# Kernel optimization log

Hardware: AMD Instinct MI355X
Metric: run time of the kernel (lower is better)

## Reference

```python
import jax, jax.numpy as jnp
import numpy as np

N_NODES = 50000
N_EDGES = 800000
IN_FEATS = 128
OUT_CLASSES = 128


def _glorot(key, shape):
    fan_in, fan_out = shape[1], shape[0]
    limit = float(np.sqrt(6.0 / (fan_in + fan_out)))
    return jax.random.uniform(key, shape, jnp.float32, -limit, limit)


def setup_inputs() -> dict:
    key = jax.random.key(0)
    ks = jax.random.split(key, 11)
    x = jax.random.normal(ks[0], (N_NODES, IN_FEATS), jnp.float32)
    edge_index = jax.random.randint(ks[1], (2, N_EDGES), 0, N_NODES, jnp.int64)
    h = OUT_CLASSES // 2
    # PyG SAGEConv: lin_l applied to aggregated neighbors (has bias), lin_r to root (no bias)
    return {
        "x": x,
        "edge_index": edge_index,
        "W_l1": _glorot(ks[2], (OUT_CLASSES, IN_FEATS)),
        "b1": jnp.zeros((OUT_CLASSES,), jnp.float32),
        "W_r1": _glorot(ks[3], (OUT_CLASSES, IN_FEATS)),
        "W_l2": _glorot(ks[4], (h, OUT_CLASSES)),
        "b2": jnp.zeros((h,), jnp.float32),
        "W_r2": _glorot(ks[5], (h, OUT_CLASSES)),
        "W_l3": _glorot(ks[6], (OUT_CLASSES, h)),
        "b3": jnp.zeros((OUT_CLASSES,), jnp.float32),
        "W_r3": _glorot(ks[7], (OUT_CLASSES, h)),
    }


def _sage_conv(x, src, dst, W_l, b, W_r):
    # gather source-node features, mean-aggregate at destinations
    msgs = x[src]                                               # [E, d]
    agg = jax.ops.segment_sum(msgs, dst, num_segments=N_NODES)  # [N, d]
    cnt = jax.ops.segment_sum(jnp.ones((src.shape[0], 1), x.dtype), dst,
                              num_segments=N_NODES)             # [N, 1]
    mean = agg / jnp.maximum(cnt, 1.0)
    return mean @ W_l.T + b + x @ W_r.T


def reference(x, edge_index, W_l1, b1, W_r1, W_l2, b2, W_r2, W_l3, b3, W_r3):
    src, dst = edge_index[0], edge_index[1]
    h = _sage_conv(x, src, dst, W_l1, b1, W_r1)
    h = _sage_conv(h, src, dst, W_l2, b2, W_r2)
    h = _sage_conv(h, src, dst, W_l3, b3, W_r3)
    return h
```

## Files before the change

kernel.cpp:

```cpp
#include <hip/hip_runtime.h>

#define N_NODES 50000
#define N_EDGES 800000
#define BUCKETS 196
#define ECHUNK 4096
#define EBLKS 196
#define BCAP 5120

typedef __attribute__((ext_vector_type(8))) _Float16 half8;
typedef __attribute__((ext_vector_type(4))) float f32x4;


__global__ __launch_bounds__(256) void prep_k(
    const int* __restrict__ src, const int* __restrict__ dst,
    int* __restrict__ gcur, unsigned* __restrict__ binned,
    const float* __restrict__ x, _Float16* __restrict__ xh,
    const float* __restrict__ Wl1, const float* __restrict__ Wr1,
    const float* __restrict__ Wl2, const float* __restrict__ Wr2,
    const float* __restrict__ Wl3, const float* __restrict__ Wr3,
    _Float16* ph_l1, _Float16* pl_l1, _Float16* ph_r1, _Float16* pl_r1,
    _Float16* ph_c2, _Float16* pl_c2, _Float16* ph_l3, _Float16* pl_l3,
    _Float16* ph_r3, _Float16* pl_r3) {
  int blk = blockIdx.x;
  int t = threadIdx.x;
  if (blk < EBLKS) {
    __shared__ int h[BUCKETS];
    __shared__ int base[BUCKETS];
    for (int i = t; i < BUCKETS; i += 256) h[i] = 0;
    __syncthreads();
    int e0 = blk * ECHUNK;
    int eend = e0 + ECHUNK < N_EDGES ? e0 + ECHUNK : N_EDGES;
    for (int e = e0 + t; e < eend; e += 256) atomicAdd(&h[dst[e] >> 8], 1);
    __syncthreads();
    for (int i = t; i < BUCKETS; i += 256) {
      if (h[i]) base[i] = atomicAdd(&gcur[i], h[i]);
      h[i] = 0;
    }
    __syncthreads();
    for (int e = e0 + t; e < eend; e += 256) {
      int d = dst[e];
      int b = d >> 8;
      int r = atomicAdd(&h[b], 1);
      binned[(size_t)b * BCAP + base[b] + r] =
          (unsigned)src[e] | ((unsigned)(d & 255) << 16);
    }
  } else if (blk < EBLKS + 32) {
    int g = (blk - EBLKS) * 256 + t;
    const float *S0, *S1 = nullptr;
    _Float16 *ph, *pl;
    int f, K;
    if (g < 2048)      { f = g;        ph = ph_l1; pl = pl_l1; S0 = Wl1; K = 128; }
    else if (g < 4096) { f = g - 2048; ph = ph_r1; pl = pl_r1; S0 = Wr1; K = 128; }
    else if (g < 6144) { f = g - 4096; ph = ph_c2; pl = pl_c2; S0 = Wl2; S1 = Wr2; K = 128; }
    else if (g < 7168) { f = g - 6144; ph = ph_l3; pl = pl_l3; S0 = Wl3; K = 64; }
    else               { f = g - 7168; ph = ph_r3; pl = pl_r3; S0 = Wr3; K = 64; }
    int kb = f >> 9;
    int rem = f & 511;
    int n = rem >> 2;
    int lq = rem & 3;
    const float* srow =
        (S1 && n >= 64) ? (S1 + (size_t)(n - 64) * K) : (S0 + (size_t)n * K);
    int kbase = kb * 32 + lq * 8;
#pragma unroll
    for (int j = 0; j < 8; ++j) {
      float v = srow[kbase + j];
      _Float16 hi = (_Float16)v;
      ph[f * 8 + j] = hi;
      pl[f * 8 + j] = (_Float16)(v - (float)hi);
    }
  } else {
    int i = (blk - EBLKS - 32) * 256 + t;
    if (i >= N_NODES * 16) return;
    const float4* xp = (const float4*)x;
    float4 a = xp[2 * i];
    float4 b = xp[2 * i + 1];
    half8 hh;
    hh[0] = (_Float16)a.x; hh[1] = (_Float16)a.y; hh[2] = (_Float16)a.z; hh[3] = (_Float16)a.w;
    hh[4] = (_Float16)b.x; hh[5] = (_Float16)b.y; hh[6] = (_Float16)b.z; hh[7] = (_Float16)b.w;
    ((half8*)xh)[i] = hh;
  }
}

__global__ __launch_bounds__(256) void bucket_fill_k(const unsigned* __restrict__ binned,
                                                     const int* __restrict__ gcnt,
                                                     int* __restrict__ offs,
                                                     int* __restrict__ deg,
                                                     unsigned short* __restrict__ csr) {
  __shared__ int cnt[256];
  __shared__ int loc[256];
  __shared__ int cur[256];
  int b = blockIdx.x;
  int t = threadIdx.x;
  int base = b * BCAP;
  int end = base + gcnt[b];
  cnt[t] = 0;
  __syncthreads();
  for (int e = base + t; e < end; e += 256) atomicAdd(&cnt[(binned[e] >> 16) & 255], 1);
  __syncthreads();
  loc[t] = cnt[t];
  __syncthreads();
  for (int o = 1; o < 256; o <<= 1) {
    int v = (t >= o) ? loc[t - o] : 0;
    __syncthreads();
    loc[t] += v;
    __syncthreads();
  }
  int excl = loc[t] - cnt[t];
  int node = b * 256 + t;
  if (node < N_NODES) {
    offs[node] = base + excl;
    deg[node] = cnt[t];
  }
  cur[t] = excl;
  __syncthreads();
  for (int e = base + t; e < end; e += 256) {
    unsigned r = binned[e];
    int dl = (r >> 16) & 255;
    int p = atomicAdd(&cur[dl], 1);
    csr[base + p] = (unsigned short)(r & 0xFFFF);
  }
}


template <int D, bool FUSE>
__global__ __launch_bounds__(256) void agg_f16_k(const _Float16* __restrict__ in,
                                                 _Float16* __restrict__ out,
                                                 const int* __restrict__ offs,
                                                 const int* __restrict__ deg,
                                                 const unsigned short* __restrict__ csr,
                                                 const float* __restrict__ bias,
                                                 const _Float16* __restrict__ addend) {
  constexpr int L = D / 8;
  constexpr int NPB = 256 / L;
  int node = blockIdx.x * NPB + threadIdx.x / L;
  int lane = threadIdx.x & (L - 1);
  if (node >= N_NODES) return;
  int start = offs[node];
  int d = deg[node];
  const half8* ip = (const half8*)in;
  float acc[8];
#pragma unroll
  for (int j = 0; j < 8; ++j) acc[j] = 0.f;
  int e = 0;
  for (; e + 8 <= d; e += 8) {
    int s[8];
#pragma unroll
    for (int j = 0; j < 8; ++j) s[j] = csr[start + e + j];
    half8 v[8];
#pragma unroll
    for (int j = 0; j < 8; ++j) v[j] = ip[(size_t)s[j] * L + lane];
#pragma unroll
    for (int j = 0; j < 8; ++j)
#pragma unroll
      for (int q = 0; q < 8; ++q) acc[q] += (float)v[j][q];
  }
  for (; e + 4 <= d; e += 4) {
    int s[4];
#pragma unroll
    for (int j = 0; j < 4; ++j) s[j] = csr[start + e + j];
    half8 v[4];
#pragma unroll
    for (int j = 0; j < 4; ++j) v[j] = ip[(size_t)s[j] * L + lane];
#pragma unroll
    for (int j = 0; j < 4; ++j)
#pragma unroll
      for (int q = 0; q < 8; ++q) acc[q] += (float)v[j][q];
  }
  for (; e < d; ++e) {
    half8 v0 = ip[(size_t)csr[start + e] * L + lane];
#pragma unroll
    for (int q = 0; q < 8; ++q) acc[q] += (float)v0[q];
  }
  float inv = d > 0 ? 1.0f / (float)d : 0.0f;
  half8 o;
  if constexpr (FUSE) {
    half8 av = ((const half8*)addend)[(size_t)node * L + lane];
#pragma unroll
    for (int q = 0; q < 8; ++q)
      o[q] = (_Float16)(acc[q] * inv + bias[lane * 8 + q] + (float)av[q]);
  } else {
#pragma unroll
    for (int q = 0; q < 8; ++q) o[q] = (_Float16)(acc[q] * inv);
  }
  ((half8*)out)[(size_t)node * L + lane] = o;
}


template <int K, bool DUAL, bool SPLIT, bool OUT32>
__global__ __launch_bounds__(256, 2) void gemm_f16_k(
    const _Float16* __restrict__ A1, const _Float16* __restrict__ W1h,
    const _Float16* __restrict__ W1l,
    const _Float16* __restrict__ A2, const _Float16* __restrict__ W2h,
    const _Float16* __restrict__ W2l,
    const float* __restrict__ bias, _Float16* __restrict__ C16,
    float* __restrict__ C32, _Float16* __restrict__ O2) {
  int wave = threadIdx.x >> 6;
  int lane = threadIdx.x & 63;
  int l15 = lane & 15;
  int lq = lane >> 4;
  int rowblk = blockIdx.x >> 1;
  int colg = blockIdx.x & 1;
  int rg = rowblk * 4 + wave;
  if (rg >= N_NODES / 16) return;
  int row0 = rg << 4;
  constexpr int KB = K / 32;
  constexpr int NN = 128;
  const int woff = (l15 * 4 + lq) * 8;
  f32x4 acc[4];
#pragma unroll
  for (int c = 0; c < 4; ++c) acc[c] = (f32x4){0.f, 0.f, 0.f, 0.f};

  constexpr int NOP = DUAL ? 2 : 1;
#pragma unroll
  for (int op = 0; op < NOP; ++op) {
    const _Float16* A = op ? A2 : A1;
    const _Float16* Wh = op ? W2h : W1h;
    const _Float16* Wl = op ? W2l : W1l;
    const _Float16* ab = A + (size_t)(row0 + l15) * K + lq * 8;
    half8 af[KB];
#pragma unroll
    for (int kb = 0; kb < KB; ++kb) af[kb] = *(const half8*)(ab + kb * 32);
#pragma unroll
    for (int kb = 0; kb < KB; ++kb) {
#pragma unroll
      for (int ct = 0; ct < 4; ++ct) {
        int n0 = colg * 64 + ct * 16;
        size_t base = (size_t)(kb * NN + n0) * 32 + woff;
        half8 bh = *(const half8*)(Wh + base);
        half8 bl = *(const half8*)(Wl + base);
        acc[ct] = __builtin_amdgcn_mfma_f32_16x16x32_f16(af[kb], bh, acc[ct], 0, 0, 0);
        acc[ct] = __builtin_amdgcn_mfma_f32_16x16x32_f16(af[kb], bl, acc[ct], 0, 0, 0);
      }
    }
  }
#pragma unroll
  for (int r = 0; r < 4; ++r) {
    int row = row0 + lq * 4 + r;
#pragma unroll
    for (int ct = 0; ct < 4; ++ct) {
      int col = colg * 64 + ct * 16 + l15;
      float v = acc[ct][r];
      if constexpr (SPLIT) {
        if (col < 64)
          C16[(size_t)row * 64 + col] = (_Float16)v;
        else
          O2[(size_t)row * 64 + (col - 64)] = (_Float16)v;
      } else {
        v += bias[col];
        if constexpr (OUT32)
          C32[(size_t)row * 128 + col] = v;
        else
          C16[(size_t)row * 128 + col] = (_Float16)v;
      }
    }
  }
}

extern "C" void kernel_launch(void* const* d_in, const int* in_sizes, int n_in,
                              void* d_out, int out_size, void* d_ws, size_t ws_size,
                              hipStream_t stream) {
  const float* x   = (const float*)d_in[0];
  const int* ei    = (const int*)d_in[1];
  const float* Wl1 = (const float*)d_in[2];
  const float* b1  = (const float*)d_in[3];
  const float* Wr1 = (const float*)d_in[4];
  const float* Wl2 = (const float*)d_in[5];
  const float* b2  = (const float*)d_in[6];
  const float* Wr2 = (const float*)d_in[7];
  const float* Wl3 = (const float*)d_in[8];
  const float* b3  = (const float*)d_in[9];
  const float* Wr3 = (const float*)d_in[10];
  float* out = (float*)d_out;

  const int* src = ei;
  const int* dst = ei + N_EDGES;

  char* ws = (char*)d_ws;
  size_t off = 0;
  auto take = [&](size_t bytes) {
    void* p = ws + off;
    off += (bytes + 255) & ~(size_t)255;
    return p;
  };
  int* deg    = (int*)take((size_t)N_NODES * 4);
  int* offs   = (int*)take((size_t)N_NODES * 4);
  int* gcur   = (int*)take((size_t)BUCKETS * 4);
  unsigned* binned = (unsigned*)take((size_t)BUCKETS * BCAP * 4);
  unsigned short* csr = (unsigned short*)take((size_t)BUCKETS * BCAP * 2);
  _Float16* xh  = (_Float16*)take((size_t)N_NODES * 128 * 2);
  _Float16* m1h = (_Float16*)take((size_t)N_NODES * 128 * 2);
  _Float16* h1h = (_Float16*)take((size_t)N_NODES * 128 * 2);
  _Float16* Ph  = (_Float16*)take((size_t)N_NODES * 64 * 2);
  _Float16* Rh  = (_Float16*)take((size_t)N_NODES * 64 * 2);
  _Float16* h2h = (_Float16*)take((size_t)N_NODES * 64 * 2);
  _Float16* m3h = (_Float16*)take((size_t)N_NODES * 64 * 2);
  _Float16* ph_l1 = (_Float16*)take(16384 * 2);
  _Float16* pl_l1 = (_Float16*)take(16384 * 2);
  _Float16* ph_r1 = (_Float16*)take(16384 * 2);
  _Float16* pl_r1 = (_Float16*)take(16384 * 2);
  _Float16* ph_c2 = (_Float16*)take(16384 * 2);
  _Float16* pl_c2 = (_Float16*)take(16384 * 2);
  _Float16* ph_l3 = (_Float16*)take(8192 * 2);
  _Float16* pl_l3 = (_Float16*)take(8192 * 2);
  _Float16* ph_r3 = (_Float16*)take(8192 * 2);
  _Float16* pl_r3 = (_Float16*)take(8192 * 2);

  const int gg = 1564;

  hipMemsetAsync(gcur, 0, (size_t)BUCKETS * 4, stream);

  prep_k<<<EBLKS + 32 + 3125, 256, 0, stream>>>(
      src, dst, gcur, binned, x, xh, Wl1, Wr1, Wl2, Wr2, Wl3, Wr3, ph_l1, pl_l1,
      ph_r1, pl_r1, ph_c2, pl_c2, ph_l3, pl_l3, ph_r3, pl_r3);
  bucket_fill_k<<<BUCKETS, 256, 0, stream>>>(binned, gcur, offs, deg, csr);

  agg_f16_k<128, false><<<3125, 256, 0, stream>>>(xh, m1h, offs, deg, csr, nullptr, nullptr);
  gemm_f16_k<128, true, false, false><<<gg, 256, 0, stream>>>(
      m1h, ph_l1, pl_l1, xh, ph_r1, pl_r1, b1, h1h, nullptr, nullptr);

  gemm_f16_k<128, false, true, false><<<gg, 256, 0, stream>>>(
      h1h, ph_c2, pl_c2, nullptr, nullptr, nullptr, nullptr, Ph, nullptr, Rh);
  agg_f16_k<64, true><<<1563, 256, 0, stream>>>(Ph, h2h, offs, deg, csr, b2, Rh);

  agg_f16_k<64, false><<<1563, 256, 0, stream>>>(h2h, m3h, offs, deg, csr, nullptr, nullptr);
  gemm_f16_k<64, true, false, true><<<gg, 256, 0, stream>>>(
      m3h, ph_l3, pl_l3, h2h, ph_r3, pl_r3, b3, nullptr, out, nullptr);
}
```

Baseline: 259.2 us.

## Fuse mean aggregation into the following GEMM via shared-memory tiles for layers 1 and 3

Adds a kernel that aggregates neighbor features for a 64-node tile into LDS and then runs the dual MFMA GEMM (aggregated and root operands) for all 128 output columns in the same block. This replaces the separate aggregation kernel and GEMM kernel for layers 1 and 3, removing the m1h/m3h intermediate round-trips through global memory and two launches. In exchange, each block does gather-heavy work followed by compute, with fewer blocks (782) and less latency hiding than the separate kernels. Each wave now also computes all 128 columns rather than splitting columns across two blocks.

```diff
diff --git a/kernel.cpp b/kernel.cpp
--- a/kernel.cpp
+++ b/kernel.cpp
@@ -186,6 +186,139 @@
 }
 
 
+template <int K, bool OUT32>
+__global__ __launch_bounds__(256, 4) void fused_agg_gemm_k(
+    const _Float16* __restrict__ feat,
+    const int* __restrict__ offs, const int* __restrict__ deg,
+    const unsigned short* __restrict__ csr,
+    const _Float16* __restrict__ Wlh, const _Float16* __restrict__ Wll,
+    const _Float16* __restrict__ Wrh, const _Float16* __restrict__ Wrl,
+    const float* __restrict__ bias, _Float16* __restrict__ C16,
+    float* __restrict__ C32) {
+  constexpr int L = K / 8;
+  constexpr int CONC = 256 / L;
+  constexpr int ITER = 64 / CONC;
+  constexpr int STRIDE = K + 8;
+  constexpr int KB = K / 32;
+  __shared__ _Float16 Asm[64 * STRIDE];
+  int t = threadIdx.x;
+  int base = blockIdx.x * 64;
+  const half8* ip = (const half8*)feat;
+  {
+    int lane = t & (L - 1);
+    int slot = t / L;
+#pragma unroll
+    for (int it = 0; it < ITER; ++it) {
+      int r = it * CONC + slot;
+      int node = base + r;
+      float acc[8];
+#pragma unroll
+      for (int j = 0; j < 8; ++j) acc[j] = 0.f;
+      float inv = 0.f;
+      if (node < N_NODES) {
+        int start = offs[node];
+        int d = deg[node];
+        int e = 0;
+        for (; e + 8 <= d; e += 8) {
+          int s[8];
+#pragma unroll
+          for (int j = 0; j < 8; ++j) s[j] = csr[start + e + j];
+          half8 v[8];
+#pragma unroll
+          for (int j = 0; j < 8; ++j) v[j] = ip[(size_t)s[j] * L + lane];
+#pragma unroll
+          for (int j = 0; j < 8; ++j)
+#pragma unroll
+            for (int q = 0; q < 8; ++q) acc[q] += (float)v[j][q];
+        }
+        for (; e + 4 <= d; e += 4) {
+          int s[4];
+#pragma unroll
+          for (int j = 0; j < 4; ++j) s[j] = csr[start + e + j];
+          half8 v[4];
+#pragma unroll
+          for (int j = 0; j < 4; ++j) v[j] = ip[(size_t)s[j] * L + lane];
+#pragma unroll
+          for (int j = 0; j < 4; ++j)
+#pragma unroll
+            for (int q = 0; q < 8; ++q) acc[q] += (float)v[j][q];
+        }
+        for (; e < d; ++e) {
+          half8 v0 = ip[(size_t)csr[start + e] * L + lane];
+#pragma unroll
+          for (int q = 0; q < 8; ++q) acc[q] += (float)v0[q];
+        }
+        inv = d > 0 ? 1.0f / (float)d : 0.0f;
+      }
+      half8 o;
+#pragma unroll
+      for (int q = 0; q < 8; ++q) o[q] = (_Float16)(acc[q] * inv);
+      *(half8*)&Asm[r * STRIDE + lane * 8] = o;
+    }
+  }
+  __syncthreads();
+  int wave = t >> 6;
+  int lane = t & 63;
+  int l15 = lane & 15;
+  int lq = lane >> 4;
+  int row0 = base + wave * 16;
+  const int woff = (l15 * 4 + lq) * 8;
+  f32x4 acc[8];
+#pragma unroll
+  for (int c = 0; c < 8; ++c) acc[c] = (f32x4){0.f, 0.f, 0.f, 0.f};
+  {
+    const _Float16* asrc = &Asm[(wave * 16 + l15) * STRIDE + lq * 8];
+    half8 af[KB];
+#pragma unroll
+    for (int kb = 0; kb < KB; ++kb) af[kb] = *(const half8*)(asrc + kb * 32);
+#pragma unroll
+    for (int kb = 0; kb < KB; ++kb) {
+#pragma unroll
+      for (int ct = 0; ct < 8; ++ct) {
+        size_t bi = (size_t)(kb * 128 + ct * 16) * 32 + woff;
+        half8 bh = *(const half8*)(Wlh + bi);
+        half8 bl = *(const half8*)(Wll + bi);
+        acc[ct] = __builtin_amdgcn_mfma_f32_16x16x32_f16(af[kb], bh, acc[ct], 0, 0, 0);
+        acc[ct] = __builtin_amdgcn_mfma_f32_16x16x32_f16(af[kb], bl, acc[ct], 0, 0, 0);
+      }
+    }
+  }
+  {
+    int arow = row0 + l15;
+    if (arow >= N_NODES) arow = N_NODES - 1;
+    const _Float16* ab = feat + (size_t)arow * K + lq * 8;
+    half8 af[KB];
+#pragma unroll
+    for (int kb = 0; kb < KB; ++kb) af[kb] = *(const half8*)(ab + kb * 32);
+#pragma unroll
+    for (int kb = 0; kb < KB; ++kb) {
+#pragma unroll
+      for (int ct = 0; ct < 8; ++ct) {
+        size_t bi = (size_t)(kb * 128 + ct * 16) * 32 + woff;
+        half8 bh = *(const half8*)(Wrh + bi);
+        half8 bl = *(const half8*)(Wrl + bi);
+        acc[ct] = __builtin_amdgcn_mfma_f32_16x16x32_f16(af[kb], bh, acc[ct], 0, 0, 0);
+        acc[ct] = __builtin_amdgcn_mfma_f32_16x16x32_f16(af[kb], bl, acc[ct], 0, 0, 0);
+      }
+    }
+  }
+#pragma unroll
+  for (int r = 0; r < 4; ++r) {
+    int row = row0 + lq * 4 + r;
+    if (row >= N_NODES) continue;
+#pragma unroll
+    for (int ct = 0; ct < 8; ++ct) {
+      int col = ct * 16 + l15;
+      float v = acc[ct][r] + bias[col];
+      if constexpr (OUT32)
+        C32[(size_t)row * 128 + col] = v;
+      else
+        C16[(size_t)row * 128 + col] = (_Float16)v;
+    }
+  }
+}
+
+
 template <int K, bool DUAL, bool SPLIT, bool OUT32>
 __global__ __launch_bounds__(256, 2) void gemm_f16_k(
     const _Float16* __restrict__ A1, const _Float16* __restrict__ W1h,
@@ -209,7 +342,6 @@
   f32x4 acc[4];
 #pragma unroll
   for (int c = 0; c < 4; ++c) acc[c] = (f32x4){0.f, 0.f, 0.f, 0.f};
-
   constexpr int NOP = DUAL ? 2 : 1;
 #pragma unroll
   for (int op = 0; op < NOP; ++op) {
@@ -288,12 +420,10 @@
   unsigned* binned = (unsigned*)take((size_t)BUCKETS * BCAP * 4);
   unsigned short* csr = (unsigned short*)take((size_t)BUCKETS * BCAP * 2);
   _Float16* xh  = (_Float16*)take((size_t)N_NODES * 128 * 2);
-  _Float16* m1h = (_Float16*)take((size_t)N_NODES * 128 * 2);
   _Float16* h1h = (_Float16*)take((size_t)N_NODES * 128 * 2);
   _Float16* Ph  = (_Float16*)take((size_t)N_NODES * 64 * 2);
   _Float16* Rh  = (_Float16*)take((size_t)N_NODES * 64 * 2);
   _Float16* h2h = (_Float16*)take((size_t)N_NODES * 64 * 2);
-  _Float16* m3h = (_Float16*)take((size_t)N_NODES * 64 * 2);
   _Float16* ph_l1 = (_Float16*)take(16384 * 2);
   _Float16* pl_l1 = (_Float16*)take(16384 * 2);
   _Float16* ph_r1 = (_Float16*)take(16384 * 2);
@@ -305,8 +435,6 @@
   _Float16* ph_r3 = (_Float16*)take(8192 * 2);
   _Float16* pl_r3 = (_Float16*)take(8192 * 2);
 
-  const int gg = 1564;
-
   hipMemsetAsync(gcur, 0, (size_t)BUCKETS * 4, stream);
 
   prep_k<<<EBLKS + 32 + 3125, 256, 0, stream>>>(
@@ -314,15 +442,13 @@
       ph_r1, pl_r1, ph_c2, pl_c2, ph_l3, pl_l3, ph_r3, pl_r3);
   bucket_fill_k<<<BUCKETS, 256, 0, stream>>>(binned, gcur, offs, deg, csr);
 
-  agg_f16_k<128, false><<<3125, 256, 0, stream>>>(xh, m1h, offs, deg, csr, nullptr, nullptr);
-  gemm_f16_k<128, true, false, false><<<gg, 256, 0, stream>>>(
-      m1h, ph_l1, pl_l1, xh, ph_r1, pl_r1, b1, h1h, nullptr, nullptr);
-
-  gemm_f16_k<128, false, true, false><<<gg, 256, 0, stream>>>(
+  fused_agg_gemm_k<128, false><<<782, 256, 0, stream>>>(
+      xh, offs, deg, csr, ph_l1, pl_l1, ph_r1, pl_r1, b1, h1h, nullptr);
+
+  gemm_f16_k<128, false, true, false><<<1564, 256, 0, stream>>>(
       h1h, ph_c2, pl_c2, nullptr, nullptr, nullptr, nullptr, Ph, nullptr, Rh);
   agg_f16_k<64, true><<<1563, 256, 0, stream>>>(Ph, h2h, offs, deg, csr, b2, Rh);
 
-  agg_f16_k<64, false><<<1563, 256, 0, stream>>>(h2h, m3h, offs, deg, csr, nullptr, nullptr);
-  gemm_f16_k<64, true, false, true><<<gg, 256, 0, stream>>>(
-      m3h, ph_l3, pl_l3, h2h, ph_r3, pl_r3, b3, nullptr, out, nullptr);
-}
+  fused_agg_gemm_k<64, true><<<782, 256, 0, stream>>>(
+      h2h, offs, deg, csr, ph_l3, pl_l3, ph_r3, pl_r3, b3, nullptr, out);
+}
```

After: 255.5 us. No clear change (-1.4%).
